# Kernel tuning notes

Measured on AMD Instinct MI355X. Metric: run time of the kernel, lower is better.

The kernel has to match this reference:

```python
import jax, jax.numpy as jnp
import numpy as np


def setup_inputs() -> dict:
    key = jax.random.key(0)
    ks = jax.random.split(key, 8)
    B, N, C = 8, 4096, 128
    x = jax.random.normal(ks[0], (B, N, C), dtype=jnp.float32)
    spatial_pos = jax.random.randint(ks[1], (1, N, N), 0, 6, dtype=jnp.int32)
    sc = 1.0 / np.sqrt(C)
    W1 = jax.random.normal(ks[2], (C, C), dtype=jnp.float32) * sc
    b1 = jax.random.normal(ks[3], (C,), dtype=jnp.float32) * 0.01
    W2 = jax.random.normal(ks[4], (C, C // 8), dtype=jnp.float32) * sc
    b2 = jax.random.normal(ks[5], (C // 8,), dtype=jnp.float32) * 0.01
    Wb = jax.random.normal(ks[6], (C + C // 8, C), dtype=jnp.float32) * (1.0 / np.sqrt(C + C // 8))
    bb = jax.random.normal(ks[7], (C,), dtype=jnp.float32) * 0.01
    return {"x": x, "spatial_pos": spatial_pos, "W1": W1, "b1": b1,
            "W2": W2, "b2": b2, "Wb": Wb, "bb": bb}


def reference(x, spatial_pos, W1, b1, W2, b2, Wb, bb):
    # s=1, l=2: scale k=1 uses mask (spatial_pos <= 1), k=2 uses (spatial_pos == 2)
    sp = spatial_pos[0]                      # [N, N], batch-invariant
    m1 = (sp <= 1).astype(x.dtype)           # [N, N]
    m2 = (sp == 2).astype(x.dtype)           # [N, N]
    h1 = x @ W1 + b1                         # [B, N, C]
    h2 = x @ W2 + b2                         # [B, N, C//8]
    # torch.bmm(mask.expand(B,-1,-1), h) == einsum over shared mask
    f1 = jnp.einsum('ij,bjc->bic', m1, h1)   # [B, N, C]
    f2 = jnp.einsum('ij,bjc->bic', m2, h2)   # [B, N, C//8]
    feats = jnp.concatenate([f1, f2], axis=-1)  # [B, N, C + C//8]
    return feats @ Wb + bb                   # [B, N, output_dim]
```

## Files before the change

kernel.cpp:

```cpp
#include <hip/hip_runtime.h>
#include <stdint.h>

typedef unsigned short u16;
typedef __attribute__((ext_vector_type(8))) short short8;
typedef __attribute__((ext_vector_type(4))) float f32x4;

#define MFMA __builtin_amdgcn_mfma_f32_16x16x32_bf16

__device__ __forceinline__ u16 f2bf(float f) {
  union { float f; uint32_t u; } v; v.f = f;
  return (u16)((v.u + 0x7FFFu + ((v.u >> 16) & 1u)) >> 16);
}

#define GLOAD16(gp, lp) \
  __builtin_amdgcn_global_load_lds((const __attribute__((address_space(1))) uint32_t*)(gp), \
                                   (__attribute__((address_space(3))) uint32_t*)(lp), 16, 0, 0)

#define WS_H    0
#define WS_Q1   9502720
#define WS_Q2   9503232
#define WS_M1P  9503744
#define WS_M2P  11600896
#define WS_RS1  13698048
#define WS_RS2  13714432
#define WS_WSB  13730816

__global__ __launch_bounds__(256) void k0(const int* __restrict__ sp,
                                          unsigned long long* __restrict__ m1p,
                                          unsigned long long* __restrict__ m2p,
                                          float* __restrict__ rs1, float* __restrict__ rs2,
                                          const float* __restrict__ W1, const float* __restrict__ Wb,
                                          const float* __restrict__ b1, const float* __restrict__ b2,
                                          const float* __restrict__ W2,
                                          float* __restrict__ q1, float* __restrict__ q2,
                                          u16* __restrict__ wsbg) {
  const int tid = threadIdx.x;
  if (blockIdx.x < 1024) {
    int wave = tid >> 6, lane = tid & 63;
    int i = blockIdx.x * 4 + wave;
    const int* rowp = sp + (size_t)i * 4096;
    int c1 = 0, c2 = 0;
    for (int w = 0; w < 64; ++w) {
      int v = rowp[w * 64 + lane];
      unsigned long long bb1 = __ballot(v <= 1);
      unsigned long long bb2 = __ballot(v == 2);
      if (lane == 0) {
        m1p[(size_t)w * 4096 + i] = bb1;
        m2p[(size_t)w * 4096 + i] = bb2;
        c1 += __popcll(bb1);
        c2 += __popcll(bb2);
      }
    }
    if (lane == 0) { rs1[i] = (float)c1; rs2[i] = (float)c2; }
    return;
  }
  int idx = (int)(blockIdx.x - 1024) * 256 + tid;
  int a = idx >> 7, c = idx & 127;
  float acc = 0.f;
  for (int k = 0; k < 128; ++k) acc += W1[a * 128 + k] * Wb[k * 128 + c];
  wsbg[(((a >> 3) * 144) + c) * 8 + (a & 7)] = f2bf(acc);
  if (idx < 2048) {
    int k = idx >> 4, nn2 = idx & 15;
    wsbg[(((k >> 3) * 144) + 128 + nn2) * 8 + (k & 7)] = f2bf(W2[k * 16 + nn2]);
  }
  if (idx < 128) {
    float s1 = 0.f, s2 = 0.f;
    for (int k = 0; k < 128; ++k) s1 += b1[k] * Wb[k * 128 + idx];
    for (int k = 0; k < 16; ++k)  s2 += b2[k] * Wb[(128 + k) * 128 + idx];
    q1[idx] = s1; q2[idx] = s2;
  }
}

__global__ __launch_bounds__(512, 1) void kproj(const float* __restrict__ x,
                                                const u16* __restrict__ wsbg,
                                                u16* __restrict__ H) {
  __shared__ u16 wsb[18432];
  __shared__ u16 xs[128 * 136];
  __shared__ u16 hs[128 * 146];
  const int tid = threadIdx.x;
  const int bid = blockIdx.x;
  const int r0 = bid * 128;
  const int b = bid >> 5;
  const int kt0 = (bid & 31) * 2;

  {
    const int e0 = tid * 8;
    GLOAD16(wsbg + e0,         (char*)&wsb[0] + e0 * 2);
    GLOAD16(wsbg + 4096 + e0,  (char*)&wsb[0] + (4096 + e0) * 2);
    GLOAD16(wsbg + 8192 + e0,  (char*)&wsb[0] + (8192 + e0) * 2);
    GLOAD16(wsbg + 12288 + e0, (char*)&wsb[0] + (12288 + e0) * 2);
    if (tid < 256)
      GLOAD16(wsbg + 16384 + e0, (char*)&wsb[0] + (16384 + e0) * 2);
  }
  {
    const float* xp = x + ((size_t)(r0 + (tid >> 2))) * 128 + (tid & 3) * 32;
    u16* xd = xs + (tid >> 2) * 136 + (tid & 3) * 32;
#pragma unroll
    for (int i = 0; i < 4; ++i) {
      f32x4 a = ((const f32x4*)xp)[i * 2];
      f32x4 bq = ((const f32x4*)xp)[i * 2 + 1];
      short8 pk;
      pk[0] = (short)f2bf(a[0]); pk[1] = (short)f2bf(a[1]);
      pk[2] = (short)f2bf(a[2]); pk[3] = (short)f2bf(a[3]);
      pk[4] = (short)f2bf(bq[0]); pk[5] = (short)f2bf(bq[1]);
      pk[6] = (short)f2bf(bq[2]); pk[7] = (short)f2bf(bq[3]);
      *(short8*)(xd + i * 8) = pk;
    }
  }
  __syncthreads();

  const int w = tid >> 6, l = tid & 63, lr = l & 15, lg = l >> 4;
  f32x4 acc[9];
  f32x4 zz = {0.f, 0.f, 0.f, 0.f};
#pragma unroll
  for (int fn = 0; fn < 9; ++fn) acc[fn] = zz;
#pragma unroll
  for (int kf = 0; kf < 4; ++kf) {
    short8 af = *(const short8*)(xs + (w * 16 + lr) * 136 + kf * 32 + lg * 8);
#pragma unroll
    for (int fn = 0; fn < 9; ++fn) {
      short8 bf = *(const short8*)(wsb + (((kf * 4 + lg) * 144) + fn * 16 + lr) * 8);
      acc[fn] = MFMA(af, bf, acc[fn], 0, 0, 0);
    }
  }
  __syncthreads();
#pragma unroll
  for (int fn = 0; fn < 9; ++fn)
#pragma unroll
    for (int g = 0; g < 4; ++g)
      hs[(w * 16 + lg * 4 + g) * 146 + fn * 16 + lr] = f2bf(acc[fn][g]);
  __syncthreads();
  for (int i = 0; i < 5; ++i) {
    int e = i * 512 + tid;
    if (e < 2304) {
      int slab = e / 1152, rem = e % 1152;
      int jbl = rem / 144, n = rem % 144;
      union { u16 s[8]; uint4 v; } pk;
#pragma unroll
      for (int r = 0; r < 8; ++r) pk.s[r] = hs[(slab * 64 + jbl * 8 + r) * 146 + n];
      int kf = jbl >> 2, lgw = jbl & 3, fn = n >> 4, lrw = n & 15;
      size_t di = ((((size_t)(kt0 + slab) * 2 + kf) * 8 + b) * 9 + fn) * 512 + (lgw * 16 + lrw) * 8;
      *(uint4*)(H + di) = pk.v;
    }
  }
}

__device__ __forceinline__ short8 expand_byte(uint32_t wd, int lgsh) {
  uint32_t b = (wd >> lgsh) & 0xFFu;
  uint32_t t = b * 0x8001u;
  union { uint32_t u[4]; short8 s; } r;
  r.u[0] = (t & 0x00010001u) * 0x3F80u;
  r.u[1] = (t & 0x00040004u) * 0x0FE0u;
  r.u[2] = (t & 0x00100010u) * 0x03F8u;
  r.u[3] = (t & 0x00400040u) * 0x00FEu;
  return r.s;
}

__global__ __launch_bounds__(512, 4) void kb1(const u16* __restrict__ H,
                                              const char* __restrict__ M1b,
                                              const char* __restrict__ M2b,
                                              const float* __restrict__ rs1, const float* __restrict__ rs2,
                                              const float* __restrict__ q1, const float* __restrict__ q2,
                                              const float* __restrict__ Wb, const float* __restrict__ bb,
                                              float* __restrict__ out) {
  __shared__ u16 bt[3][9216];
  __shared__ u16 mkb[3][512];
  __shared__ float f2pf[2][64][16];
  __shared__ u16 f2s[64 * 40];
  __shared__ u16 wb2s[4096];

  const int tid = threadIdx.x;
  const int bid = blockIdx.x;
  const int b = bid & 7;
  const int i0 = (bid >> 3) * 64;

  const int w = tid >> 6, l = tid & 63, lr = l & 15, lg = l >> 4;
  const int g = w >> 2, c = w & 3;
  const int fm2 = w & 3, kf2 = w >> 2;
  const int lgsh = lg * 8;

  const int e0 = tid * 8, e1 = 4096 + tid * 8, e2 = 8192 + tid * 8;
  const uint32_t soff0 = b * 4608 + e0;
  const uint32_t soff1 = b * 4608 + (uint32_t)(e1 < 4608 ? e1 : 32256 + e1);
  const uint32_t soff2 = b * 4608 + 32256 + e2;
  const char* mksrc = ((tid < 32) ? M1b : M2b) + (size_t)i0 * 8 + (size_t)(tid & 31) * 16;

#define STAGE(P, BUF) { \
    const u16* hp_ = H + (size_t)(P) * 73728; \
    GLOAD16(hp_ + soff0, (char*)&bt[BUF][0] + e0 * 2); \
    GLOAD16(hp_ + soff1, (char*)&bt[BUF][0] + e1 * 2); \
    if (tid < 128) GLOAD16(hp_ + soff2, (char*)&bt[BUF][0] + e2 * 2); \
    if (tid < 64)  GLOAD16(mksrc + (size_t)(P) * 32768, (char*)&mkb[BUF][0] + tid * 16); }

  const int fA0 = (c * 2 + 0) * 512 + l * 8;
  const int fA1 = (c * 2 + 1) * 512 + l * 8;
  const int fB0 = 4608 + fA0;
  const int fB1 = 4608 + fA1;
  const int fM  = kf2 * 4608 + 8 * 512 + l * 8;

  f32x4 zz = {0.f, 0.f, 0.f, 0.f};
  f32x4 acc00 = zz, acc01 = zz, acc10 = zz, acc11 = zz;
  f32x4 acc2 = zz;

#define WAITV { if (w == 0) asm volatile("s_waitcnt vmcnt(4)" ::: "memory"); \
                else if (w == 1) asm volatile("s_waitcnt vmcnt(3)" ::: "memory"); \
                else asm volatile("s_waitcnt vmcnt(2)" ::: "memory"); }

#define COMPUTE(BUF) { \
    const u16* src_ = &bt[BUF][0]; \
    uint2 c0_ = *(const uint2*)&mkb[BUF][((g * 2 + 0) * 16 + lr) * 4]; \
    uint2 c1_ = *(const uint2*)&mkb[BUF][((g * 2 + 1) * 16 + lr) * 4]; \
    uint32_t c2_ = *(const uint32_t*)&mkb[BUF][256 + (fm2 * 16 + lr) * 4 + kf2 * 2]; \
    short8 bA0_ = *(const short8*)(src_ + fA0); \
    short8 bA1_ = *(const short8*)(src_ + fA1); \
    short8 bB0_ = *(const short8*)(src_ + fB0); \
    short8 bB1_ = *(const short8*)(src_ + fB1); \
    short8 bM_  = *(const short8*)(src_ + fM); \
    short8 e0x_ = expand_byte(c0_.x, lgsh), e0y_ = expand_byte(c0_.y, lgsh); \
    short8 e1x_ = expand_byte(c1_.x, lgsh), e1y_ = expand_byte(c1_.y, lgsh); \
    short8 e2v_ = expand_byte(c2_, lgsh); \
    __builtin_amdgcn_s_setprio(1); \
    acc00 = MFMA(e0x_, bA0_, acc00, 0, 0, 0); \
    acc01 = MFMA(e0x_, bA1_, acc01, 0, 0, 0); \
    acc00 = MFMA(e0y_, bB0_, acc00, 0, 0, 0); \
    acc01 = MFMA(e0y_, bB1_, acc01, 0, 0, 0); \
    acc10 = MFMA(e1x_, bA0_, acc10, 0, 0, 0); \
    acc11 = MFMA(e1x_, bA1_, acc11, 0, 0, 0); \
    acc10 = MFMA(e1y_, bB0_, acc10, 0, 0, 0); \
    acc11 = MFMA(e1y_, bB1_, acc11, 0, 0, 0); \
    acc2  = MFMA(e2v_, bM_, acc2, 0, 0, 0); \
    __builtin_amdgcn_s_setprio(0); }

#define PHASE(P, BUF, BUF2) { WAITV; __builtin_amdgcn_s_barrier(); \
    STAGE((P) + 2, BUF2); COMPUTE(BUF) }

  STAGE(0, 0);
  STAGE(1, 1);

#pragma unroll
  for (int i = 0; i < 8; ++i) {
    int e = i * 512 + tid;
    int r_ = e & 7, nn = (e >> 3) & 127, jb = e >> 10;
    int k = jb * 8 + r_;
    wb2s[e] = f2bf((k < 16) ? Wb[(128 + k) * 128 + nn] : 0.f);
  }

  for (int p = 0; p < 60; p += 3) {
    PHASE(p, 0, 2);
    PHASE(p + 1, 1, 0);
    PHASE(p + 2, 2, 1);
  }
  PHASE(60, 0, 2);
  PHASE(61, 1, 0);
  { WAITV; __builtin_amdgcn_s_barrier(); COMPUTE(2) }
  { asm volatile("s_waitcnt vmcnt(0)" ::: "memory");
    __builtin_amdgcn_s_barrier(); COMPUTE(0) }

#pragma unroll
  for (int gg = 0; gg < 4; ++gg)
    f2pf[kf2][fm2 * 16 + lg * 4 + gg][lr] = acc2[gg];
  __syncthreads();
#pragma unroll
  for (int j = 0; j < 2; ++j) {
    int e = j * 512 + tid;
    int row = e >> 4, col = e & 15;
    f2s[row * 40 + col] = f2bf(f2pf[0][row][col] + f2pf[1][row][col]);
    f2s[row * 40 + 16 + col] = 0;
  }
  __syncthreads();

  short8 bw0 = *(const short8*)(wb2s + ((lg * 128) + (c * 2 + 0) * 16 + lr) * 8);
  short8 bw1 = *(const short8*)(wb2s + ((lg * 128) + (c * 2 + 1) * 16 + lr) * 8);
  {
    short8 af0 = *(const short8*)(f2s + ((g * 2 + 0) * 16 + lr) * 40 + lg * 8);
    short8 af1 = *(const short8*)(f2s + ((g * 2 + 1) * 16 + lr) * 40 + lg * 8);
    acc00 = MFMA(af0, bw0, acc00, 0, 0, 0);
    acc01 = MFMA(af0, bw1, acc01, 0, 0, 0);
    acc10 = MFMA(af1, bw0, acc10, 0, 0, 0);
    acc11 = MFMA(af1, bw1, acc11, 0, 0, 0);
  }

  const int col0 = (c * 2 + 0) * 16 + lr, col1 = (c * 2 + 1) * 16 + lr;
  const float q10 = q1[col0], q20 = q2[col0], bb0 = bb[col0];
  const float q11 = q1[col1], q21 = q2[col1], bb1 = bb[col1];
#pragma unroll
  for (int i = 0; i < 2; ++i) {
    f32x4 a0 = i ? acc10 : acc00;
    f32x4 a1 = i ? acc11 : acc01;
#pragma unroll
    for (int gg = 0; gg < 4; ++gg) {
      int row = (g * 2 + i) * 16 + lg * 4 + gg;
      float r1 = rs1[i0 + row], r2 = rs2[i0 + row];
      size_t obase = ((size_t)b * 4096 + i0 + row) * 128;
      out[obase + col0] = a0[gg] + r1 * q10 + r2 * q20 + bb0;
      out[obase + col1] = a1[gg] + r1 * q11 + r2 * q21 + bb1;
    }
  }
}

extern "C" void kernel_launch(void* const* d_in, const int* in_sizes, int n_in,
                              void* d_out, int out_size, void* d_ws, size_t ws_size,
                              hipStream_t stream) {
  const float* x  = (const float*)d_in[0];
  const int*   sp = (const int*)d_in[1];
  const float* W1 = (const float*)d_in[2];
  const float* b1 = (const float*)d_in[3];
  const float* W2 = (const float*)d_in[4];
  const float* b2 = (const float*)d_in[5];
  const float* Wb = (const float*)d_in[6];
  const float* bb = (const float*)d_in[7];
  float* out = (float*)d_out;
  char* ws = (char*)d_ws;

  u16* H = (u16*)(ws + WS_H);
  float* q1 = (float*)(ws + WS_Q1);
  float* q2 = (float*)(ws + WS_Q2);
  unsigned long long* m1p = (unsigned long long*)(ws + WS_M1P);
  unsigned long long* m2p = (unsigned long long*)(ws + WS_M2P);
  float* rs1 = (float*)(ws + WS_RS1);
  float* rs2 = (float*)(ws + WS_RS2);
  u16* wsbg = (u16*)(ws + WS_WSB);

  k0<<<1088, 256, 0, stream>>>(sp, m1p, m2p, rs1, rs2, W1, Wb, b1, b2, W2, q1, q2, wsbg);
  kproj<<<256, 512, 0, stream>>>(x, wsbg, H);
  kb1<<<512, 512, 0, stream>>>(H, (const char*)m1p, (const char*)m2p,
                               rs1, rs2, q1, q2, Wb, bb, out);
}
```

Measured before the change: 92.43 us.

## Fuse mask packing and projection into one kernel, recompute W1·Wb per block

Merges the mask-packing/weight-prep kernel and the projection kernel into a single launch. Each projection block now recomputes the fused W1·Wb weight with MFMA in shared memory instead of reading a precomputed global buffer. This removes one kernel launch and the serial dependency between the two stages, letting mask packing run alongside the projection. The cost is redundant per-block weight recomputation, extra barriers, and a strided bf16 conversion of Wb in every projection block.

```diff
diff --git a/kernel.cpp b/kernel.cpp
--- a/kernel.cpp
+++ b/kernel.cpp
@@ -11,10 +11,6 @@
   union { float f; uint32_t u; } v; v.f = f;
   return (u16)((v.u + 0x7FFFu + ((v.u >> 16) & 1u)) >> 16);
 }
-
-#define GLOAD16(gp, lp) \
-  __builtin_amdgcn_global_load_lds((const __attribute__((address_space(1))) uint32_t*)(gp), \
-                                   (__attribute__((address_space(3))) uint32_t*)(lp), 16, 0, 0)
 
 #define WS_H    0
 #define WS_Q1   9502720
@@ -23,75 +19,118 @@
 #define WS_M2P  11600896
 #define WS_RS1  13698048
 #define WS_RS2  13714432
-#define WS_WSB  13730816
-
-__global__ __launch_bounds__(256) void k0(const int* __restrict__ sp,
-                                          unsigned long long* __restrict__ m1p,
-                                          unsigned long long* __restrict__ m2p,
-                                          float* __restrict__ rs1, float* __restrict__ rs2,
-                                          const float* __restrict__ W1, const float* __restrict__ Wb,
-                                          const float* __restrict__ b1, const float* __restrict__ b2,
-                                          const float* __restrict__ W2,
-                                          float* __restrict__ q1, float* __restrict__ q2,
-                                          u16* __restrict__ wsbg) {
+
+#define GLOAD16(gp, lp) \
+  __builtin_amdgcn_global_load_lds((const __attribute__((address_space(1))) uint32_t*)(gp), \
+                                   (__attribute__((address_space(3))) uint32_t*)(lp), 16, 0, 0)
+
+__global__ __launch_bounds__(512, 1) void kpre(const float* __restrict__ x,
+                                               const int* __restrict__ sp,
+                                               const float* __restrict__ W1,
+                                               const float* __restrict__ b1,
+                                               const float* __restrict__ W2,
+                                               const float* __restrict__ b2,
+                                               const float* __restrict__ Wb,
+                                               u16* __restrict__ H,
+                                               unsigned long long* __restrict__ m1p,
+                                               unsigned long long* __restrict__ m2p,
+                                               float* __restrict__ rs1, float* __restrict__ rs2,
+                                               float* __restrict__ q1, float* __restrict__ q2) {
   const int tid = threadIdx.x;
-  if (blockIdx.x < 1024) {
-    int wave = tid >> 6, lane = tid & 63;
-    int i = blockIdx.x * 4 + wave;
-    const int* rowp = sp + (size_t)i * 4096;
-    int c1 = 0, c2 = 0;
-    for (int w = 0; w < 64; ++w) {
-      int v = rowp[w * 64 + lane];
-      unsigned long long bb1 = __ballot(v <= 1);
-      unsigned long long bb2 = __ballot(v == 2);
-      if (lane == 0) {
-        m1p[(size_t)w * 4096 + i] = bb1;
-        m2p[(size_t)w * 4096 + i] = bb2;
-        c1 += __popcll(bb1);
-        c2 += __popcll(bb2);
+  const int bid = blockIdx.x;
+
+  if (bid >= 256) {
+    if (bid < 768) {
+      int wave = tid >> 6, lane = tid & 63;
+      int i = (bid - 256) * 8 + wave;
+      const int* rowp = sp + (size_t)i * 4096;
+      int c1 = 0, c2 = 0;
+      for (int w = 0; w < 64; ++w) {
+        int v = rowp[w * 64 + lane];
+        unsigned long long bb1 = __ballot(v <= 1);
+        unsigned long long bb2 = __ballot(v == 2);
+        if (lane == 0) {
+          m1p[(size_t)w * 4096 + i] = bb1;
+          m2p[(size_t)w * 4096 + i] = bb2;
+          c1 += __popcll(bb1);
+          c2 += __popcll(bb2);
+        }
       }
-    }
-    if (lane == 0) { rs1[i] = (float)c1; rs2[i] = (float)c2; }
+      if (lane == 0) { rs1[i] = (float)c1; rs2[i] = (float)c2; }
+    } else if (tid < 128) {
+      float s1 = 0.f, s2 = 0.f;
+      for (int k = 0; k < 128; ++k) s1 += b1[k] * Wb[k * 128 + tid];
+      for (int k = 0; k < 16; ++k)  s2 += b2[k] * Wb[(128 + k) * 128 + tid];
+      q1[tid] = s1; q2[tid] = s2;
+    }
     return;
   }
-  int idx = (int)(blockIdx.x - 1024) * 256 + tid;
-  int a = idx >> 7, c = idx & 127;
-  float acc = 0.f;
-  for (int k = 0; k < 128; ++k) acc += W1[a * 128 + k] * Wb[k * 128 + c];
-  wsbg[(((a >> 3) * 144) + c) * 8 + (a & 7)] = f2bf(acc);
-  if (idx < 2048) {
-    int k = idx >> 4, nn2 = idx & 15;
-    wsbg[(((k >> 3) * 144) + 128 + nn2) * 8 + (k & 7)] = f2bf(W2[k * 16 + nn2]);
-  }
-  if (idx < 128) {
-    float s1 = 0.f, s2 = 0.f;
-    for (int k = 0; k < 128; ++k) s1 += b1[k] * Wb[k * 128 + idx];
-    for (int k = 0; k < 16; ++k)  s2 += b2[k] * Wb[(128 + k) * 128 + idx];
-    q1[idx] = s1; q2[idx] = s2;
-  }
-}
-
-__global__ __launch_bounds__(512, 1) void kproj(const float* __restrict__ x,
-                                                const u16* __restrict__ wsbg,
-                                                u16* __restrict__ H) {
+
   __shared__ u16 wsb[18432];
   __shared__ u16 xs[128 * 136];
   __shared__ u16 hs[128 * 146];
-  const int tid = threadIdx.x;
-  const int bid = blockIdx.x;
   const int r0 = bid * 128;
   const int b = bid >> 5;
   const int kt0 = (bid & 31) * 2;
-
-  {
-    const int e0 = tid * 8;
-    GLOAD16(wsbg + e0,         (char*)&wsb[0] + e0 * 2);
-    GLOAD16(wsbg + 4096 + e0,  (char*)&wsb[0] + (4096 + e0) * 2);
-    GLOAD16(wsbg + 8192 + e0,  (char*)&wsb[0] + (8192 + e0) * 2);
-    GLOAD16(wsbg + 12288 + e0, (char*)&wsb[0] + (12288 + e0) * 2);
-    if (tid < 256)
-      GLOAD16(wsbg + 16384 + e0, (char*)&wsb[0] + (16384 + e0) * 2);
-  }
+  const int w = tid >> 6, l = tid & 63, lr = l & 15, lg = l >> 4;
+
+  {
+    const float* wp = W1 + ((size_t)(tid >> 2)) * 128 + (tid & 3) * 32;
+    u16* wd = xs + (tid >> 2) * 136 + (tid & 3) * 32;
+#pragma unroll
+    for (int i = 0; i < 4; ++i) {
+      f32x4 a = ((const f32x4*)wp)[i * 2];
+      f32x4 bq = ((const f32x4*)wp)[i * 2 + 1];
+      short8 pk;
+      pk[0] = (short)f2bf(a[0]); pk[1] = (short)f2bf(a[1]);
+      pk[2] = (short)f2bf(a[2]); pk[3] = (short)f2bf(a[3]);
+      pk[4] = (short)f2bf(bq[0]); pk[5] = (short)f2bf(bq[1]);
+      pk[6] = (short)f2bf(bq[2]); pk[7] = (short)f2bf(bq[3]);
+      *(short8*)(wd + i * 8) = pk;
+    }
+  }
+  {
+    u16* wbs = hs;
+    for (int i = 0; i < 32; ++i) {
+      int e = i * 512 + tid;
+      int k = e >> 7, c = e & 127;
+      wbs[(((k >> 3) * 128) + c) * 8 + (k & 7)] = f2bf(Wb[k * 128 + c]);
+    }
+  }
+  {
+    for (int i = 0; i < 4; ++i) {
+      int e = i * 512 + tid;
+      int k = e >> 4, nn = e & 15;
+      wsb[(((k >> 3) * 144) + 128 + nn) * 8 + (k & 7)] = f2bf(W2[k * 16 + nn]);
+    }
+  }
+  __syncthreads();
+
+  {
+    f32x4 accp[8];
+    f32x4 zz = {0.f, 0.f, 0.f, 0.f};
+#pragma unroll
+    for (int fn = 0; fn < 8; ++fn) accp[fn] = zz;
+#pragma unroll
+    for (int kf = 0; kf < 4; ++kf) {
+      short8 af = *(const short8*)(xs + (w * 16 + lr) * 136 + kf * 32 + lg * 8);
+#pragma unroll
+      for (int fn = 0; fn < 8; ++fn) {
+        short8 bf = *(const short8*)(hs + (((kf * 4 + lg) * 128) + fn * 16 + lr) * 8);
+        accp[fn] = MFMA(af, bf, accp[fn], 0, 0, 0);
+      }
+    }
+    __syncthreads();
+#pragma unroll
+    for (int fn = 0; fn < 8; ++fn)
+#pragma unroll
+      for (int g = 0; g < 4; ++g) {
+        int a = w * 16 + lg * 4 + g;
+        int c = fn * 16 + lr;
+        wsb[(((a >> 3) * 144) + c) * 8 + (a & 7)] = f2bf(accp[fn][g]);
+      }
+  }
+  __syncthreads();
   {
     const float* xp = x + ((size_t)(r0 + (tid >> 2))) * 128 + (tid & 3) * 32;
     u16* xd = xs + (tid >> 2) * 136 + (tid & 3) * 32;
@@ -109,7 +148,6 @@
   }
   __syncthreads();
 
-  const int w = tid >> 6, l = tid & 63, lr = l & 15, lg = l >> 4;
   f32x4 acc[9];
   f32x4 zz = {0.f, 0.f, 0.f, 0.f};
 #pragma unroll
@@ -319,10 +357,8 @@
   unsigned long long* m2p = (unsigned long long*)(ws + WS_M2P);
   float* rs1 = (float*)(ws + WS_RS1);
   float* rs2 = (float*)(ws + WS_RS2);
-  u16* wsbg = (u16*)(ws + WS_WSB);
-
-  k0<<<1088, 256, 0, stream>>>(sp, m1p, m2p, rs1, rs2, W1, Wb, b1, b2, W2, q1, q2, wsbg);
-  kproj<<<256, 512, 0, stream>>>(x, wsbg, H);
+
+  kpre<<<769, 512, 0, stream>>>(x, sp, W1, b1, W2, b2, Wb, H, m1p, m2p, rs1, rs2, q1, q2);
   kb1<<<512, 512, 0, stream>>>(H, (const char*)m1p, (const char*)m2p,
                                rs1, rs2, q1, q2, Wb, bb, out);
 }
```

Measured after the change: 111.4 us. +20.6%, slower.

## Double kb1 block to 128 rows with 1024 threads to share H tiles

Applied to the files above, without the earlier changes.

The kb1 mask-aggregation kernel now gives each block 128 output rows and 1024 threads instead of 64 rows and 512 threads, and the grid is halved. Each staged H tile in LDS is reused by twice as many rows, which cuts global and LDS load traffic per output. The staging code is simplified to use pointers that advance each phase, and the vmcnt waits are adjusted to the new load counts. In exchange, the triple-buffered barriers now span 16 waves, and the block count drops to one per CU.

```diff
diff --git a/kernel.cpp b/kernel.cpp
--- a/kernel.cpp
+++ b/kernel.cpp
@@ -156,61 +156,64 @@
   return r.s;
 }
 
-__global__ __launch_bounds__(512, 4) void kb1(const u16* __restrict__ H,
-                                              const char* __restrict__ M1b,
-                                              const char* __restrict__ M2b,
-                                              const float* __restrict__ rs1, const float* __restrict__ rs2,
-                                              const float* __restrict__ q1, const float* __restrict__ q2,
-                                              const float* __restrict__ Wb, const float* __restrict__ bb,
-                                              float* __restrict__ out) {
+__global__ __launch_bounds__(1024, 4) void kb1(const u16* __restrict__ H,
+                                               const char* __restrict__ M1b,
+                                               const char* __restrict__ M2b,
+                                               const float* __restrict__ rs1, const float* __restrict__ rs2,
+                                               const float* __restrict__ q1, const float* __restrict__ q2,
+                                               const float* __restrict__ Wb, const float* __restrict__ bb,
+                                               float* __restrict__ out) {
   __shared__ u16 bt[3][9216];
-  __shared__ u16 mkb[3][512];
-  __shared__ float f2pf[2][64][16];
-  __shared__ u16 f2s[64 * 40];
+  __shared__ u16 mkb[3][1024];
+  __shared__ float f2pf[2][128][16];
+  __shared__ u16 f2s[128 * 40];
   __shared__ u16 wb2s[4096];
 
   const int tid = threadIdx.x;
   const int bid = blockIdx.x;
   const int b = bid & 7;
-  const int i0 = (bid >> 3) * 64;
+  const int i0 = (bid >> 3) * 128;
 
   const int w = tid >> 6, l = tid & 63, lr = l & 15, lg = l >> 4;
   const int g = w >> 2, c = w & 3;
-  const int fm2 = w & 3, kf2 = w >> 2;
+  const int fm2 = w & 7, kf2 = w >> 3;
   const int lgsh = lg * 8;
 
-  const int e0 = tid * 8, e1 = 4096 + tid * 8, e2 = 8192 + tid * 8;
-  const uint32_t soff0 = b * 4608 + e0;
-  const uint32_t soff1 = b * 4608 + (uint32_t)(e1 < 4608 ? e1 : 32256 + e1);
-  const uint32_t soff2 = b * 4608 + 32256 + e2;
-  const char* mksrc = ((tid < 32) ? M1b : M2b) + (size_t)i0 * 8 + (size_t)(tid & 31) * 16;
-
-#define STAGE(P, BUF) { \
-    const u16* hp_ = H + (size_t)(P) * 73728; \
-    GLOAD16(hp_ + soff0, (char*)&bt[BUF][0] + e0 * 2); \
-    GLOAD16(hp_ + soff1, (char*)&bt[BUF][0] + e1 * 2); \
-    if (tid < 128) GLOAD16(hp_ + soff2, (char*)&bt[BUF][0] + e2 * 2); \
-    if (tid < 64)  GLOAD16(mksrc + (size_t)(P) * 32768, (char*)&mkb[BUF][0] + tid * 16); }
+  const uint32_t cA = tid, cB = 1024 + tid;
+  const uint32_t offA = (cA < 576) ? (b * 4608 + cA * 8) : (36864 + b * 4608 + (cA - 576) * 8);
+  const uint32_t offB = 36864 + b * 4608 + (cB - 576) * 8;
+  const u16* pB1 = H + offA;
+  const u16* pB2 = H + offB;
+  const char* pM = (((tid & 64) ? M2b : M1b)) + (size_t)i0 * 8 + (size_t)(tid & 63) * 16;
+  const int d1 = tid * 16;
+  const int d2 = 16384 + tid * 16;
+  const int dM = (tid - 128) * 16;
+
+#define STAGE(BUF) { \
+    GLOAD16(pB1, (char*)&bt[BUF][0] + d1); \
+    if (tid < 128) GLOAD16(pB2, (char*)&bt[BUF][0] + d2); \
+    else if (tid < 256) GLOAD16(pM, (char*)&mkb[BUF][0] + dM); \
+    pB1 += 73728; pB2 += 73728; pM += 32768; }
 
   const int fA0 = (c * 2 + 0) * 512 + l * 8;
   const int fA1 = (c * 2 + 1) * 512 + l * 8;
   const int fB0 = 4608 + fA0;
   const int fB1 = 4608 + fA1;
-  const int fM  = kf2 * 4608 + 8 * 512 + l * 8;
+  const int fM  = kf2 * 4608 + 4096 + l * 8;
 
   f32x4 zz = {0.f, 0.f, 0.f, 0.f};
   f32x4 acc00 = zz, acc01 = zz, acc10 = zz, acc11 = zz;
   f32x4 acc2 = zz;
 
-#define WAITV { if (w == 0) asm volatile("s_waitcnt vmcnt(4)" ::: "memory"); \
-                else if (w == 1) asm volatile("s_waitcnt vmcnt(3)" ::: "memory"); \
-                else asm volatile("s_waitcnt vmcnt(2)" ::: "memory"); }
+#define WAITV { if (w < 4) asm volatile("s_waitcnt vmcnt(2)" ::: "memory"); \
+                else asm volatile("s_waitcnt vmcnt(1)" ::: "memory"); }
 
 #define COMPUTE(BUF) { \
     const u16* src_ = &bt[BUF][0]; \
-    uint2 c0_ = *(const uint2*)&mkb[BUF][((g * 2 + 0) * 16 + lr) * 4]; \
-    uint2 c1_ = *(const uint2*)&mkb[BUF][((g * 2 + 1) * 16 + lr) * 4]; \
-    uint32_t c2_ = *(const uint32_t*)&mkb[BUF][256 + (fm2 * 16 + lr) * 4 + kf2 * 2]; \
+    const char* mk_ = (const char*)&mkb[BUF][0]; \
+    uint2 c0_ = *(const uint2*)(mk_ + ((g * 2 + 0) * 16 + lr) * 8); \
+    uint2 c1_ = *(const uint2*)(mk_ + ((g * 2 + 1) * 16 + lr) * 8); \
+    uint32_t c2_ = *(const uint32_t*)(mk_ + 1024 + (fm2 * 16 + lr) * 8 + kf2 * 4); \
     short8 bA0_ = *(const short8*)(src_ + fA0); \
     short8 bA1_ = *(const short8*)(src_ + fA1); \
     short8 bB0_ = *(const short8*)(src_ + fB0); \
@@ -231,27 +234,26 @@
     acc2  = MFMA(e2v_, bM_, acc2, 0, 0, 0); \
     __builtin_amdgcn_s_setprio(0); }
 
-#define PHASE(P, BUF, BUF2) { WAITV; __builtin_amdgcn_s_barrier(); \
-    STAGE((P) + 2, BUF2); COMPUTE(BUF) }
-
-  STAGE(0, 0);
-  STAGE(1, 1);
-
-#pragma unroll
-  for (int i = 0; i < 8; ++i) {
-    int e = i * 512 + tid;
+#define PHASE(BUF, BUF2) { WAITV; __builtin_amdgcn_s_barrier(); STAGE(BUF2); COMPUTE(BUF) }
+
+  STAGE(0);
+  STAGE(1);
+
+#pragma unroll
+  for (int i = 0; i < 4; ++i) {
+    int e = i * 1024 + tid;
     int r_ = e & 7, nn = (e >> 3) & 127, jb = e >> 10;
     int k = jb * 8 + r_;
     wb2s[e] = f2bf((k < 16) ? Wb[(128 + k) * 128 + nn] : 0.f);
   }
 
-  for (int p = 0; p < 60; p += 3) {
-    PHASE(p, 0, 2);
-    PHASE(p + 1, 1, 0);
-    PHASE(p + 2, 2, 1);
-  }
-  PHASE(60, 0, 2);
-  PHASE(61, 1, 0);
+  for (int it = 0; it < 20; ++it) {
+    PHASE(0, 2);
+    PHASE(1, 0);
+    PHASE(2, 1);
+  }
+  PHASE(0, 2);
+  PHASE(1, 0);
   { WAITV; __builtin_amdgcn_s_barrier(); COMPUTE(2) }
   { asm volatile("s_waitcnt vmcnt(0)" ::: "memory");
     __builtin_amdgcn_s_barrier(); COMPUTE(0) }
@@ -262,7 +264,7 @@
   __syncthreads();
 #pragma unroll
   for (int j = 0; j < 2; ++j) {
-    int e = j * 512 + tid;
+    int e = j * 1024 + tid;
     int row = e >> 4, col = e & 15;
     f2s[row * 40 + col] = f2bf(f2pf[0][row][col] + f2pf[1][row][col]);
     f2s[row * 40 + 16 + col] = 0;
@@ -323,6 +325,6 @@
 
   k0<<<1088, 256, 0, stream>>>(sp, m1p, m2p, rs1, rs2, W1, Wb, b1, b2, W2, q1, q2, wsbg);
   kproj<<<256, 512, 0, stream>>>(x, wsbg, H);
-  kb1<<<512, 512, 0, stream>>>(H, (const char*)m1p, (const char*)m2p,
-                               rs1, rs2, q1, q2, Wb, bb, out);
-}
+  kb1<<<256, 1024, 0, stream>>>(H, (const char*)m1p, (const char*)m2p,
+                                rs1, rs2, q1, q2, Wb, bb, out);
+}
```

Result: no change. 92.82 us (+0.4%).
